# Optimization experiments

Measured on AMD Instinct MI355X. Metric: run time of the kernel, lower is better.

## Reference

```python
import jax, jax.numpy as jnp
import numpy as np

FEATURE_SIZE = 3072
LSTM_IN = 1024
LSTM_HIDDEN = 1024
NUM_CLASSES = 22


def setup_inputs() -> dict:
    key = jax.random.key(0)
    ks = jax.random.split(key, 9)
    s = lambda fan: 1.0 / np.sqrt(fan)
    feature_in = jax.random.normal(ks[0], (64, 512, FEATURE_SIZE), dtype=jnp.float32)
    W_pre = jax.random.uniform(ks[1], (LSTM_IN, FEATURE_SIZE), minval=-s(FEATURE_SIZE), maxval=s(FEATURE_SIZE))
    b_pre = jax.random.uniform(ks[2], (LSTM_IN,), minval=-s(FEATURE_SIZE), maxval=s(FEATURE_SIZE))
    W_ih = jax.random.uniform(ks[3], (4 * LSTM_HIDDEN, LSTM_IN), minval=-s(LSTM_HIDDEN), maxval=s(LSTM_HIDDEN))
    b_ih = jax.random.uniform(ks[4], (4 * LSTM_HIDDEN,), minval=-s(LSTM_HIDDEN), maxval=s(LSTM_HIDDEN))
    W_hh = jax.random.uniform(ks[5], (4 * LSTM_HIDDEN, LSTM_HIDDEN), minval=-s(LSTM_HIDDEN), maxval=s(LSTM_HIDDEN))
    b_hh = jax.random.uniform(ks[6], (4 * LSTM_HIDDEN,), minval=-s(LSTM_HIDDEN), maxval=s(LSTM_HIDDEN))
    W_cls = jax.random.uniform(ks[7], (NUM_CLASSES, LSTM_HIDDEN), minval=-s(LSTM_HIDDEN), maxval=s(LSTM_HIDDEN))
    b_cls = jax.random.uniform(ks[8], (NUM_CLASSES,), minval=-s(LSTM_HIDDEN), maxval=s(LSTM_HIDDEN))
    return dict(feature_in=feature_in, W_pre=W_pre, b_pre=b_pre, W_ih=W_ih, b_ih=b_ih,
                W_hh=W_hh, b_hh=b_hh, W_cls=W_cls, b_cls=b_cls)


def reference(feature_in, W_pre, b_pre, W_ih, b_ih, W_hh, b_hh, W_cls, b_cls):
    B, T, _ = feature_in.shape
    H = LSTM_HIDDEN
    # Preprocess Linear+ReLU for all timesteps at once (no recurrence here).
    x = jax.nn.relu(jnp.einsum('btf,if->bti', feature_in, W_pre) + b_pre)  # [B,T,LSTM_IN]
    # Precompute input contribution to the gates for all steps.
    gx = jnp.einsum('bti,gi->btg', x, W_ih) + b_ih + b_hh  # [B,T,4H]
    gx = jnp.swapaxes(gx, 0, 1)  # [T,B,4H] for scan

    def step(carry, gx_t):
        h, c = carry
        gates = gx_t + h @ W_hh.T  # [B,4H]
        i, f, g, o = jnp.split(gates, 4, axis=-1)  # PyTorch LSTMCell gate order
        i, f, o = jax.nn.sigmoid(i), jax.nn.sigmoid(f), jax.nn.sigmoid(o)
        g = jnp.tanh(g)
        c = f * c + i * g
        h = o * jnp.tanh(c)
        score = h @ W_cls.T + b_cls  # dropout is identity at eval
        return (h, c), score

    init = (jnp.zeros((B, H), feature_in.dtype), jnp.zeros((B, H), feature_in.dtype))
    _, scores = jax.lax.scan(step, init, gx)  # scores: [T,B,NUM_CLASSES]
    return jnp.swapaxes(scores, 0, 1).reshape(-1, NUM_CLASSES)
```

## Files before the change

kernel.cpp:

```cpp
#include <hip/hip_runtime.h>

typedef unsigned short u16;
typedef unsigned int u32;
typedef __attribute__((ext_vector_type(8))) __bf16 bf8;
typedef __attribute__((ext_vector_type(4))) float f4;

__device__ __forceinline__ u16 f2bu(float f) {
  u32 u = __float_as_uint(f);
  u = (u + 0x7fffu + ((u >> 16) & 1u)) >> 16;
  return (u16)u;
}
__device__ __forceinline__ float b2f(u16 v) {
  return __uint_as_float(((u32)v) << 16);
}

__global__ __launch_bounds__(256) void k_f2b(const float* __restrict__ src,
                                             u16* __restrict__ dst, long n) {
  long i = ((long)blockIdx.x * 256 + threadIdx.x) * 8;
  if (i + 8 > n) return;
  float4 a = *(const float4*)(src + i);
  float4 b = *(const float4*)(src + i + 4);
  union { u16 h[8]; uint4 v; } r;
  r.h[0] = f2bu(a.x); r.h[1] = f2bu(a.y); r.h[2] = f2bu(a.z); r.h[3] = f2bu(a.w);
  r.h[4] = f2bu(b.x); r.h[5] = f2bu(b.y); r.h[6] = f2bu(b.z); r.h[7] = f2bu(b.w);
  *(uint4*)(dst + i) = r.v;
}

__global__ __launch_bounds__(256) void k_bsum(const float* __restrict__ a,
                                              const float* __restrict__ b,
                                              float* __restrict__ o, int n) {
  int i = blockIdx.x * 256 + threadIdx.x;
  if (i < n) o[i] = a[i] + b[i];
}

__global__ __launch_bounds__(256) void k_zerobar(u32* __restrict__ p) {
  for (int i = threadIdx.x; i < 4352; i += 256) p[i] = 0;
}

template<int MODE>
__global__ __launch_bounds__(256) void k_gemm(const u16* __restrict__ A, const u16* __restrict__ B,
                                              const float* __restrict__ bias, u16* __restrict__ out,
                                              int M, int N, int K)
{
  __shared__ u16 As[128][40];
  __shared__ u16 Bs[128][40];
  const int tid = threadIdx.x;
  const int bm = blockIdx.y, bn = blockIdx.x;
  const int wave = tid >> 6, lane = tid & 63;
  const int wm = wave & 1, wn = wave >> 1;
  const f4 fzero = {0.f, 0.f, 0.f, 0.f};
  f4 acc[4][4];
#pragma unroll
  for (int i = 0; i < 4; i++)
#pragma unroll
    for (int j = 0; j < 4; j++) acc[i][j] = fzero;

  const u16* Ab = A + (size_t)bm * 128 * K;
  const u16* Bb = B + (size_t)bn * 128 * K;
  const int row_s = tid >> 2;
  const int cs = (tid & 3) * 8;

  for (int k0 = 0; k0 < K; k0 += 32) {
    __syncthreads();
#pragma unroll
    for (int L = 0; L < 2; L++) {
      int row = L * 64 + row_s;
      *(uint4*)&As[row][cs] = *(const uint4*)(Ab + (size_t)row * K + k0 + cs);
      *(uint4*)&Bs[row][cs] = *(const uint4*)(Bb + (size_t)row * K + k0 + cs);
    }
    __syncthreads();
    const int kf = (lane >> 4) * 8;
    const int rr = lane & 15;
    bf8 af[4], bfr[4];
#pragma unroll
    for (int i = 0; i < 4; i++) {
      af[i]  = *(const bf8*)&As[wm * 64 + i * 16 + rr][kf];
      bfr[i] = *(const bf8*)&Bs[wn * 64 + i * 16 + rr][kf];
    }
#pragma unroll
    for (int i = 0; i < 4; i++)
#pragma unroll
      for (int j = 0; j < 4; j++)
        acc[i][j] = __builtin_amdgcn_mfma_f32_16x16x32_bf16(af[i], bfr[j], acc[i][j], 0, 0, 0);
  }
  const int mq = (lane >> 4) * 4;
  const int nn = lane & 15;
#pragma unroll
  for (int i = 0; i < 4; i++) {
#pragma unroll
    for (int j = 0; j < 4; j++) {
      int n = bn * 128 + wn * 64 + j * 16 + nn;
      float bv = bias[n];
#pragma unroll
      for (int r = 0; r < 4; r++) {
        int m = bm * 128 + wm * 64 + i * 16 + mq + r;
        float v = acc[i][j][r] + bv;
        if (MODE == 0) {
          v = fmaxf(v, 0.f);
          out[(size_t)m * N + n] = f2bu(v);
        } else {
          int t = m & 511, b = m >> 9;
          int g = n >> 10, hg = n & 1023;
          out[((size_t)t * 256 + (size_t)(b >> 4) * 64 + (hg >> 4)) * 1024
              + (size_t)g * 256 + (b & 15) * 16 + (hg & 15)] = f2bu(v);
        }
      }
    }
  }
}

__global__ __launch_bounds__(256) void k_scan(const u16* __restrict__ gx,
                                              const u16* __restrict__ Whh,
                                              u16* __restrict__ hh,
                                              u32* __restrict__ bar)
{
  extern __shared__ char smem[];
  u16*  Wl = (u16*)smem;
  u16*  hb = (u16*)(smem + 132096);
  float* gl = (float*)(smem + 148736);
  float* cl = (float*)(smem + 152832);
  const int tid = threadIdx.x, lane = tid & 63, wv = tid >> 6;
  const int bq = (blockIdx.x & 7) >> 1;
  const int hs = ((blockIdx.x >> 3) << 1) | (blockIdx.x & 1);
  u32* rel   = bar;
  u32* flags = bar + 256;

  for (int idx = tid; idx < 64 * 128; idx += 256) {
    int r = idx >> 7, s = idx & 127;
    int gr = (r >> 4) * 1024 + hs * 16 + (r & 15);
    *(uint4*)&Wl[r * 1032 + s * 8] = *(const uint4*)(Whh + (size_t)gr * 1024 + s * 8);
  }
  cl[tid] = 0.f;
  __syncthreads();

  const int kf = (lane >> 4) * 8;
  const int ra = lane & 15;
  const int rb = wv * 16 + (lane & 15);
  const int srow = tid >> 4;
  const int sseg = tid & 15;

  for (int t = 0; t < 512; t++) {
    const size_t gxo = ((size_t)t * 256 + (size_t)bq * 64 + hs) * 1024 + tid;
    u16 gxr0 = gx[gxo];
    u16 gxr1 = gx[gxo + 256];
    u16 gxr2 = gx[gxo + 512];
    u16 gxr3 = gx[gxo + 768];

    f4 acc = {0.f, 0.f, 0.f, 0.f};
    if (t > 0) {
      const u16* hp = hh + ((size_t)(t - 1) * 64 + bq * 16) * 1024;
      for (int kc = 0; kc < 1024; kc += 512) {
        __syncthreads();
#pragma unroll
        for (int u = 0; u < 4; u++) {
          int s = sseg + u * 16;
          *(uint4*)&hb[srow * 520 + s * 8] = *(const uint4*)(hp + (size_t)srow * 1024 + kc + s * 8);
        }
        __syncthreads();
#pragma unroll
        for (int k = 0; k < 512; k += 32) {
          bf8 a = *(const bf8*)&hb[ra * 520 + k + kf];
          bf8 b = *(const bf8*)&Wl[rb * 1032 + kc + k + kf];
          acc = __builtin_amdgcn_mfma_f32_16x16x32_bf16(a, b, acc, 0, 0, 0);
        }
      }
    }
    {
      int n = lane & 15, m0 = (lane >> 4) * 4;
#pragma unroll
      for (int r = 0; r < 4; r++) gl[wv * 256 + (m0 + r) * 16 + n] = acc[r];
    }
    __syncthreads();
    {
      int b = tid >> 4, hl2 = tid & 15;
      int bg = bq * 16 + b, hg = hs * 16 + hl2;
      float gi = gl[0 * 256 + tid] + b2f(gxr0);
      float gf = gl[1 * 256 + tid] + b2f(gxr1);
      float gg = gl[2 * 256 + tid] + b2f(gxr2);
      float go = gl[3 * 256 + tid] + b2f(gxr3);
      float i_ = 1.f / (1.f + __expf(-gi));
      float f_ = 1.f / (1.f + __expf(-gf));
      float g_ = 1.f - 2.f / (__expf(2.f * gg) + 1.f);
      float o_ = 1.f / (1.f + __expf(-go));
      float c = f_ * cl[tid] + i_ * g_;
      cl[tid] = c;
      float h = o_ * (1.f - 2.f / (__expf(2.f * c) + 1.f));
      hh[((size_t)t * 64 + bg) * 1024 + hg] = f2bu(h);
    }
    __syncthreads();
    if (hs == 0) {
      if (wv == 0) {
        __threadfence();
        if (lane == 0)
          __hip_atomic_store(&flags[(bq * 64) * 16], (u32)(t + 1),
                             __ATOMIC_RELAXED, __HIP_MEMORY_SCOPE_AGENT);
        const u32* fp = &flags[(bq * 64 + lane) * 16];
        while (__hip_atomic_load(fp, __ATOMIC_RELAXED,
                                 __HIP_MEMORY_SCOPE_AGENT) < (u32)(t + 1))
          __builtin_amdgcn_s_sleep(1);
        __threadfence();
        if (lane == 0)
          __hip_atomic_store(&rel[bq * 64], (u32)(t + 1),
                             __ATOMIC_RELAXED, __HIP_MEMORY_SCOPE_AGENT);
      }
    } else {
      if (tid == 0) {
        __threadfence();
        __hip_atomic_store(&flags[(bq * 64 + hs) * 16], (u32)(t + 1),
                           __ATOMIC_RELAXED, __HIP_MEMORY_SCOPE_AGENT);
        while (__hip_atomic_load(&rel[bq * 64], __ATOMIC_RELAXED,
                                 __HIP_MEMORY_SCOPE_AGENT) < (u32)(t + 1))
          __builtin_amdgcn_s_sleep(2);
        __threadfence();
      }
    }
    __syncthreads();
  }
}

__global__ __launch_bounds__(256) void k_scores(const u16* __restrict__ hh,
                                                const u16* __restrict__ Wcb,
                                                const float* __restrict__ bcls,
                                                float* __restrict__ out)
{
  __shared__ u16 Wc[22 * 1032];
  __shared__ u16 hl[8 * 1032];
  const int tid = threadIdx.x;
  for (int idx = tid; idx < 22 * 128; idx += 256) {
    int r = idx >> 7, s = idx & 127;
    *(uint4*)&Wc[r * 1032 + s * 8] = *(const uint4*)(Wcb + (size_t)r * 1024 + s * 8);
  }
  size_t row0 = (size_t)blockIdx.x * 8;
  for (int idx = tid; idx < 8 * 128; idx += 256) {
    int r = idx >> 7, s = idx & 127;
    *(uint4*)&hl[r * 1032 + s * 8] = *(const uint4*)(hh + (row0 + r) * 1024 + s * 8);
  }
  __syncthreads();
  if (tid < 176) {
    int rl = tid / 22, cls = tid % 22;
    const u16* hp = &hl[rl * 1032];
    const u16* wp = &Wc[cls * 1032];
    float acc = 0.f;
#pragma unroll 4
    for (int k = 0; k < 1024; k += 2) {
      u32 hu = *(const u32*)(hp + k);
      u32 wu = *(const u32*)(wp + k);
      float h0 = __uint_as_float(hu << 16), h1 = __uint_as_float(hu & 0xffff0000u);
      float w0 = __uint_as_float(wu << 16), w1 = __uint_as_float(wu & 0xffff0000u);
      acc += h0 * w0 + h1 * w1;
    }
    size_t r = row0 + rl;
    int t = (int)(r >> 6), b = (int)(r & 63);
    out[((size_t)b * 512 + t) * 22 + cls] = acc + bcls[cls];
  }
}

extern "C" void kernel_launch(void* const* d_in, const int* in_sizes, int n_in,
                              void* d_out, int out_size, void* d_ws, size_t ws_size,
                              hipStream_t stream)
{
  (void)in_sizes; (void)n_in; (void)out_size;
  const float* feat = (const float*)d_in[0];
  const float* Wpre = (const float*)d_in[1];
  const float* bpre = (const float*)d_in[2];
  const float* Wih  = (const float*)d_in[3];
  const float* bih  = (const float*)d_in[4];
  const float* Whh  = (const float*)d_in[5];
  const float* bhh  = (const float*)d_in[6];
  const float* Wcls = (const float*)d_in[7];
  const float* bcls = (const float*)d_in[8];
  char* ws = (char*)d_ws;

  const size_t OFF_GX   = 0;
  const size_t OFF_XB   = 268435456;
  const size_t OFF_WPRE = 335544320;
  const size_t OFF_WIH  = 341835776;
  const size_t OFF_WHH  = 350224384;
  const size_t OFF_WCLS = 358612992;
  const size_t OFF_BSUM = 358658048;
  const size_t OFF_BAR  = 358674432;
  const size_t NEED     = 358707200;
  if (ws_size < NEED) return;

  u16* featb = (u16*)(ws + OFF_GX);
  u16* gxb   = (u16*)(ws + OFF_GX);
  u16* xb    = (u16*)(ws + OFF_XB);
  u16* hhb   = (u16*)(ws + OFF_XB);
  u16* wpreb = (u16*)(ws + OFF_WPRE);
  u16* wihb  = (u16*)(ws + OFF_WIH);
  u16* whhb  = (u16*)(ws + OFF_WHH);
  u16* wclsb = (u16*)(ws + OFF_WCLS);
  float* bsum = (float*)(ws + OFF_BSUM);
  u32* barp  = (u32*)(ws + OFF_BAR);

  k_f2b<<<dim3(49152), dim3(256), 0, stream>>>(feat, featb, 100663296L);
  k_f2b<<<dim3(1536),  dim3(256), 0, stream>>>(Wpre, wpreb, 3145728L);
  k_f2b<<<dim3(2048),  dim3(256), 0, stream>>>(Wih,  wihb,  4194304L);
  k_f2b<<<dim3(2048),  dim3(256), 0, stream>>>(Whh,  whhb,  4194304L);
  k_f2b<<<dim3(11),    dim3(256), 0, stream>>>(Wcls, wclsb, 22528L);
  k_bsum<<<dim3(16),   dim3(256), 0, stream>>>(bih, bhh, bsum, 4096);
  k_zerobar<<<dim3(1), dim3(256), 0, stream>>>(barp);

  k_gemm<0><<<dim3(8, 256),  dim3(256), 0, stream>>>(featb, wpreb, bpre, xb,  32768, 1024, 3072);
  k_gemm<1><<<dim3(32, 256), dim3(256), 0, stream>>>(xb,    wihb,  bsum, gxb, 32768, 4096, 1024);

  const u16* gx_c = gxb;
  const u16* whh_c = whhb;
  u16* hh_p = hhb;
  u32* bar_p = barp;
  void* args[4] = { (void*)&gx_c, (void*)&whh_c, (void*)&hh_p, (void*)&bar_p };
  hipFuncSetAttribute((const void*)k_scan, hipFuncAttributeMaxDynamicSharedMemorySize, 153856);
  hipLaunchCooperativeKernel((void*)k_scan, dim3(256), dim3(256), args, 153856, stream);

  k_scores<<<dim3(4096), dim3(256), 0, stream>>>(hhb, wclsb, bcls, (float*)d_out);
}
```

Before: 8.022 ms.

## Replace per-step barrier with step-tagged hidden-state words for dataflow sync

Removes the two-level flag/release barrier in the LSTM scan. Each block now publishes every hidden value as a 32-bit word that packs the step number with the bf16 value, into a double-buffered global array. Consumers spin on atomic loads until all the words they need carry the expected tag, so each block waits only on the data it reads instead of on a full group barrier. The MFMA accumulation is also split into two independent accumulator chains. The cost is twice the global traffic for h, plus polling on many words per thread, which can waste bandwidth while waiting.

```diff
diff --git a/kernel.cpp b/kernel.cpp
--- a/kernel.cpp
+++ b/kernel.cpp
@@ -33,8 +33,9 @@
   if (i < n) o[i] = a[i] + b[i];
 }
 
-__global__ __launch_bounds__(256) void k_zerobar(u32* __restrict__ p) {
-  for (int i = threadIdx.x; i < 4352; i += 256) p[i] = 0;
+__global__ __launch_bounds__(256) void k_zero32(u32* __restrict__ p, int n) {
+  int i = blockIdx.x * 256 + threadIdx.x;
+  if (i < n) p[i] = 0;
 }
 
 template<int MODE>
@@ -112,7 +113,7 @@
 __global__ __launch_bounds__(256) void k_scan(const u16* __restrict__ gx,
                                               const u16* __restrict__ Whh,
                                               u16* __restrict__ hh,
-                                              u32* __restrict__ bar)
+                                              u32* __restrict__ hh32)
 {
   extern __shared__ char smem[];
   u16*  Wl = (u16*)smem;
@@ -122,8 +123,6 @@
   const int tid = threadIdx.x, lane = tid & 63, wv = tid >> 6;
   const int bq = (blockIdx.x & 7) >> 1;
   const int hs = ((blockIdx.x >> 3) << 1) | (blockIdx.x & 1);
-  u32* rel   = bar;
-  u32* flags = bar + 256;
 
   for (int idx = tid; idx < 64 * 128; idx += 256) {
     int r = idx >> 7, s = idx & 127;
@@ -146,29 +145,55 @@
     u16 gxr2 = gx[gxo + 512];
     u16 gxr3 = gx[gxo + 768];
 
-    f4 acc = {0.f, 0.f, 0.f, 0.f};
+    f4 acc0 = {0.f, 0.f, 0.f, 0.f};
+    f4 acc1 = {0.f, 0.f, 0.f, 0.f};
     if (t > 0) {
-      const u16* hp = hh + ((size_t)(t - 1) * 64 + bq * 16) * 1024;
+      const u32 tgt = (u32)t;
+      const u32* slot = hh32 + ((size_t)((t - 1) & 1) << 16);
+#pragma unroll
       for (int kc = 0; kc < 1024; kc += 512) {
         __syncthreads();
-#pragma unroll
-        for (int u = 0; u < 4; u++) {
-          int s = sseg + u * 16;
-          *(uint4*)&hb[srow * 520 + s * 8] = *(const uint4*)(hp + (size_t)srow * 1024 + kc + s * 8);
+        {
+          const u32* hp32 = slot + (size_t)(bq * 16 + srow) * 1024 + kc + sseg * 32;
+          u32 w[32];
+          for (;;) {
+            bool ok = true;
+#pragma unroll
+            for (int q = 0; q < 32; q++)
+              w[q] = __hip_atomic_load(hp32 + q, __ATOMIC_RELAXED,
+                                       __HIP_MEMORY_SCOPE_AGENT);
+#pragma unroll
+            for (int q = 0; q < 32; q++) ok &= ((w[q] >> 16) == tgt);
+            if (ok) break;
+            __builtin_amdgcn_s_sleep(1);
+          }
+#pragma unroll
+          for (int q = 0; q < 8; q++) {
+            u32 p0 = (w[q * 4 + 0] & 0xffffu) | (w[q * 4 + 1] << 16);
+            u32 p1 = (w[q * 4 + 2] & 0xffffu) | (w[q * 4 + 3] << 16);
+            *(uint2*)&hb[srow * 520 + sseg * 32 + q * 4] = make_uint2(p0, p1);
+          }
         }
         __syncthreads();
 #pragma unroll
-        for (int k = 0; k < 512; k += 32) {
+        for (int k = 0; k < 256; k += 32) {
           bf8 a = *(const bf8*)&hb[ra * 520 + k + kf];
           bf8 b = *(const bf8*)&Wl[rb * 1032 + kc + k + kf];
-          acc = __builtin_amdgcn_mfma_f32_16x16x32_bf16(a, b, acc, 0, 0, 0);
+          acc0 = __builtin_amdgcn_mfma_f32_16x16x32_bf16(a, b, acc0, 0, 0, 0);
+        }
+#pragma unroll
+        for (int k = 256; k < 512; k += 32) {
+          bf8 a = *(const bf8*)&hb[ra * 520 + k + kf];
+          bf8 b = *(const bf8*)&Wl[rb * 1032 + kc + k + kf];
+          acc1 = __builtin_amdgcn_mfma_f32_16x16x32_bf16(a, b, acc1, 0, 0, 0);
         }
       }
     }
     {
       int n = lane & 15, m0 = (lane >> 4) * 4;
 #pragma unroll
-      for (int r = 0; r < 4; r++) gl[wv * 256 + (m0 + r) * 16 + n] = acc[r];
+      for (int r = 0; r < 4; r++)
+        gl[wv * 256 + (m0 + r) * 16 + n] = acc0[r] + acc1[r];
     }
     __syncthreads();
     {
@@ -185,36 +210,12 @@
       float c = f_ * cl[tid] + i_ * g_;
       cl[tid] = c;
       float h = o_ * (1.f - 2.f / (__expf(2.f * c) + 1.f));
-      hh[((size_t)t * 64 + bg) * 1024 + hg] = f2bu(h);
-    }
-    __syncthreads();
-    if (hs == 0) {
-      if (wv == 0) {
-        __threadfence();
-        if (lane == 0)
-          __hip_atomic_store(&flags[(bq * 64) * 16], (u32)(t + 1),
-                             __ATOMIC_RELAXED, __HIP_MEMORY_SCOPE_AGENT);
-        const u32* fp = &flags[(bq * 64 + lane) * 16];
-        while (__hip_atomic_load(fp, __ATOMIC_RELAXED,
-                                 __HIP_MEMORY_SCOPE_AGENT) < (u32)(t + 1))
-          __builtin_amdgcn_s_sleep(1);
-        __threadfence();
-        if (lane == 0)
-          __hip_atomic_store(&rel[bq * 64], (u32)(t + 1),
-                             __ATOMIC_RELAXED, __HIP_MEMORY_SCOPE_AGENT);
-      }
-    } else {
-      if (tid == 0) {
-        __threadfence();
-        __hip_atomic_store(&flags[(bq * 64 + hs) * 16], (u32)(t + 1),
-                           __ATOMIC_RELAXED, __HIP_MEMORY_SCOPE_AGENT);
-        while (__hip_atomic_load(&rel[bq * 64], __ATOMIC_RELAXED,
-                                 __HIP_MEMORY_SCOPE_AGENT) < (u32)(t + 1))
-          __builtin_amdgcn_s_sleep(2);
-        __threadfence();
-      }
-    }
-    __syncthreads();
+      u16 h16 = f2bu(h);
+      hh[((size_t)t * 64 + bg) * 1024 + hg] = h16;
+      __hip_atomic_store(hh32 + ((size_t)(t & 1) << 16) + (size_t)bg * 1024 + hg,
+                         ((u32)(t + 1) << 16) | (u32)h16,
+                         __ATOMIC_RELAXED, __HIP_MEMORY_SCOPE_AGENT);
+    }
   }
 }
 
@@ -278,8 +279,8 @@
   const size_t OFF_WHH  = 350224384;
   const size_t OFF_WCLS = 358612992;
   const size_t OFF_BSUM = 358658048;
-  const size_t OFF_BAR  = 358674432;
-  const size_t NEED     = 358707200;
+  const size_t OFF_H32  = 358674432;
+  const size_t NEED     = 359198720;
   if (ws_size < NEED) return;
 
   u16* featb = (u16*)(ws + OFF_GX);
@@ -291,7 +292,7 @@
   u16* whhb  = (u16*)(ws + OFF_WHH);
   u16* wclsb = (u16*)(ws + OFF_WCLS);
   float* bsum = (float*)(ws + OFF_BSUM);
-  u32* barp  = (u32*)(ws + OFF_BAR);
+  u32* h32p  = (u32*)(ws + OFF_H32);
 
   k_f2b<<<dim3(49152), dim3(256), 0, stream>>>(feat, featb, 100663296L);
   k_f2b<<<dim3(1536),  dim3(256), 0, stream>>>(Wpre, wpreb, 3145728L);
@@ -299,7 +300,7 @@
   k_f2b<<<dim3(2048),  dim3(256), 0, stream>>>(Whh,  whhb,  4194304L);
   k_f2b<<<dim3(11),    dim3(256), 0, stream>>>(Wcls, wclsb, 22528L);
   k_bsum<<<dim3(16),   dim3(256), 0, stream>>>(bih, bhh, bsum, 4096);
-  k_zerobar<<<dim3(1), dim3(256), 0, stream>>>(barp);
+  k_zero32<<<dim3(512), dim3(256), 0, stream>>>(h32p, 131072);
 
   k_gemm<0><<<dim3(8, 256),  dim3(256), 0, stream>>>(featb, wpreb, bpre, xb,  32768, 1024, 3072);
   k_gemm<1><<<dim3(32, 256), dim3(256), 0, stream>>>(xb,    wihb,  bsum, gxb, 32768, 4096, 1024);
@@ -307,8 +308,8 @@
   const u16* gx_c = gxb;
   const u16* whh_c = whhb;
   u16* hh_p = hhb;
-  u32* bar_p = barp;
-  void* args[4] = { (void*)&gx_c, (void*)&whh_c, (void*)&hh_p, (void*)&bar_p };
+  u32* h32_p = h32p;
+  void* args[4] = { (void*)&gx_c, (void*)&whh_c, (void*)&hh_p, (void*)&h32_p };
   hipFuncSetAttribute((const void*)k_scan, hipFuncAttributeMaxDynamicSharedMemorySize, 153856);
   hipLaunchCooperativeKernel((void*)k_scan, dim3(256), dim3(256), args, 153856, stream);
 
```

Result: slower. 18.69 ms (+132.9%).
